# Performance work log

Measured on AMD Instinct MI355X. Metric: run time of the kernel, lower is better.

The kernel has to match this reference:

```python
import jax, jax.numpy as jnp
import numpy as np

EDGE_WIDTH = 64
NUM_HEADS = 8
DOT_DIM = EDGE_WIDTH // NUM_HEADS  # 8
B, N = 2, 384
LN_EPS = 1e-5


def setup_inputs() -> dict:
    key = jax.random.key(0)
    ks = jax.random.split(key, 8)
    e = jax.random.normal(ks[0], (B, N, N, EDGE_WIDTH), dtype=jnp.float32)
    mask = jnp.zeros((B, N, N, 1), dtype=jnp.float32)  # additive mask, broadcast over heads
    s = 1.0 / np.sqrt(EDGE_WIDTH)
    return {
        "e": e,
        "mask": mask,
        "ln_w": jnp.ones((EDGE_WIDTH,), jnp.float32),
        "ln_b": jnp.zeros((EDGE_WIDTH,), jnp.float32),
        "W_V": jax.random.normal(ks[1], (EDGE_WIDTH, 2 * EDGE_WIDTH), jnp.float32) * s,
        "b_V": jnp.zeros((2 * EDGE_WIDTH,), jnp.float32),
        "W_EG": jax.random.normal(ks[2], (EDGE_WIDTH, 4 * NUM_HEADS), jnp.float32) * s,
        "b_EG": jnp.zeros((4 * NUM_HEADS,), jnp.float32),
        "W_O": jax.random.normal(ks[3], (2 * EDGE_WIDTH, EDGE_WIDTH), jnp.float32) * (1.0 / np.sqrt(2 * EDGE_WIDTH)),
        "b_O": jnp.zeros((EDGE_WIDTH,), jnp.float32),
    }


def reference(e, mask, ln_w, ln_b, W_V, b_V, W_EG, b_EG, W_O, b_O):
    b, n = e.shape[0], e.shape[1]
    H, D = NUM_HEADS, DOT_DIM
    # LayerNorm over edge_width
    mu = jnp.mean(e, axis=-1, keepdims=True)
    var = jnp.mean(jnp.square(e - mu), axis=-1, keepdims=True)
    e_ln = (e - mu) * jax.lax.rsqrt(var + LN_EPS) * ln_w + ln_b

    V = e_ln @ W_V + b_V                        # [b,n,n,2*ew]
    V_in, V_out = jnp.split(V, 2, axis=-1)
    # view(..., dot_dim, num_heads): last dim splits with heads fastest
    V_in = V_in.reshape(b, n, n, D, H)
    V_out = V_out.reshape(b, n, n, D, H)

    EG = e_ln @ W_EG + b_EG                     # [b,n,n,4H]
    E_in, G_in, E_out, G_out = jnp.split(EG, 4, axis=-1)

    gates_in = jax.nn.sigmoid(G_in + mask)
    A_in = jax.nn.softmax(E_in + mask, axis=2) * gates_in      # [b,n,n,H]
    Va_in = jnp.einsum('bikh,bjkdh->bijdh', A_in, V_in)

    gates_out = jax.nn.sigmoid(G_out + mask)
    A_out = jax.nn.softmax(E_out + mask, axis=1) * gates_out   # [b,n,n,H]
    Va_out = jnp.einsum('bkih,bkjdh->bijdh', A_out, V_out)

    Va = jnp.concatenate([Va_in, Va_out], axis=-1).reshape(b, n, n, 2 * EDGE_WIDTH)
    return Va @ W_O + b_O
```

## Files before the change

### kernel.cpp

```cpp
#include <hip/hip_runtime.h>

#define N_ 384
#define LNEPS 1e-5f

typedef __attribute__((ext_vector_type(8))) short bf16x8;
typedef __attribute__((ext_vector_type(4))) float f32x4;

__device__ __forceinline__ float bf2f(unsigned int u) {
    union { unsigned int i; float f; } v; v.i = u << 16; return v.f;
}
__device__ __forceinline__ unsigned short f2bf(float f) {
    union { float f; unsigned int i; } v; v.f = f;
    return (unsigned short)((v.i + 0x7FFFu + ((v.i >> 16) & 1u)) >> 16);
}
__device__ __forceinline__ void gload16(const void* g, void* l) {
    __builtin_amdgcn_global_load_lds(
        (const __attribute__((address_space(1))) void*)g,
        (__attribute__((address_space(3))) void*)l, 16, 0, 0);
}

__global__ __launch_bounds__(256) void k0_prep(
    const float* __restrict__ W_V, const float* __restrict__ W_EG,
    unsigned short* __restrict__ Whi, unsigned short* __restrict__ Wlo)
{
    int x = blockIdx.x * 256 + threadIdx.x;
    if (x >= 10240) return;
    int col = x >> 6, k = x & 63;
    float wv = (col < 128) ? W_V[k * 128 + col] : W_EG[k * 32 + (col - 128)];
    unsigned short hi = f2bf(wv);
    Whi[x] = hi;
    Wlo[x] = f2bf(wv - bf2f(hi));
}

__global__ __launch_bounds__(256) void k1_ln_proj(
    const float* __restrict__ e, const float* __restrict__ mask,
    const float* __restrict__ ln_w, const float* __restrict__ ln_b,
    const unsigned short* __restrict__ Whi_g, const unsigned short* __restrict__ Wlo_g,
    const float* __restrict__ b_V, const float* __restrict__ b_EG,
    unsigned short* __restrict__ VtIn, unsigned short* __restrict__ VtOut,
    float* __restrict__ EGin, float* __restrict__ EGoutT)
{
    __shared__ __align__(16) char smem[25088];
    unsigned short* s_v = (unsigned short*)smem;
    float* s_eg = (float*)(smem + 16640);

    const int t = threadIdx.x;
    const int j0 = blockIdx.x * 4;
    const int i0 = blockIdx.y * 16;
    const int b  = blockIdx.z;

    const int l = t & 63, w = t >> 6;
    const int l15 = l & 15, lq = l >> 4;

    const int r = w * 16 + l15;
    const int r1f = i0 + (r >> 2), r2f = j0 + (r & 3);
    const float* erow = e + ((size_t)((b * N_ + r1f) * N_ + r2f)) * 64;
    float ev[16];
    {
        float4 e0 = *(const float4*)(erow + lq * 8);
        float4 e1 = *(const float4*)(erow + lq * 8 + 4);
        float4 e2 = *(const float4*)(erow + 32 + lq * 8);
        float4 e3 = *(const float4*)(erow + 32 + lq * 8 + 4);
        ev[0]=e0.x; ev[1]=e0.y; ev[2]=e0.z;  ev[3]=e0.w;
        ev[4]=e1.x; ev[5]=e1.y; ev[6]=e1.z;  ev[7]=e1.w;
        ev[8]=e2.x; ev[9]=e2.y; ev[10]=e2.z; ev[11]=e2.w;
        ev[12]=e3.x; ev[13]=e3.y; ev[14]=e3.z; ev[15]=e3.w;
    }
    float s = 0.f, sq = 0.f;
    #pragma unroll
    for (int j = 0; j < 16; ++j) { s += ev[j]; sq += ev[j] * ev[j]; }
    s  += __shfl_xor(s, 16);  s  += __shfl_xor(s, 32);
    sq += __shfl_xor(sq, 16); sq += __shfl_xor(sq, 32);
    const float mean = s * (1.f / 64.f);
    const float rstd = rsqrtf(sq * (1.f / 64.f) - mean * mean + LNEPS);

    bf16x8 ahi[2], alo[2];
    {
        float lnwv[16], lnbv[16];
        float4 w0 = *(const float4*)(ln_w + lq * 8);
        float4 w1 = *(const float4*)(ln_w + lq * 8 + 4);
        float4 w2 = *(const float4*)(ln_w + 32 + lq * 8);
        float4 w3 = *(const float4*)(ln_w + 32 + lq * 8 + 4);
        lnwv[0]=w0.x; lnwv[1]=w0.y; lnwv[2]=w0.z;  lnwv[3]=w0.w;
        lnwv[4]=w1.x; lnwv[5]=w1.y; lnwv[6]=w1.z;  lnwv[7]=w1.w;
        lnwv[8]=w2.x; lnwv[9]=w2.y; lnwv[10]=w2.z; lnwv[11]=w2.w;
        lnwv[12]=w3.x; lnwv[13]=w3.y; lnwv[14]=w3.z; lnwv[15]=w3.w;
        float4 b0 = *(const float4*)(ln_b + lq * 8);
        float4 b1 = *(const float4*)(ln_b + lq * 8 + 4);
        float4 b2 = *(const float4*)(ln_b + 32 + lq * 8);
        float4 b3 = *(const float4*)(ln_b + 32 + lq * 8 + 4);
        lnbv[0]=b0.x; lnbv[1]=b0.y; lnbv[2]=b0.z;  lnbv[3]=b0.w;
        lnbv[4]=b1.x; lnbv[5]=b1.y; lnbv[6]=b1.z;  lnbv[7]=b1.w;
        lnbv[8]=b2.x; lnbv[9]=b2.y; lnbv[10]=b2.z; lnbv[11]=b2.w;
        lnbv[12]=b3.x; lnbv[13]=b3.y; lnbv[14]=b3.z; lnbv[15]=b3.w;
        #pragma unroll
        for (int ks = 0; ks < 2; ++ks) {
            #pragma unroll
            for (int j = 0; j < 8; ++j) {
                float x = (ev[ks * 8 + j] - mean) * rstd * lnwv[ks * 8 + j] + lnbv[ks * 8 + j];
                unsigned short h = f2bf(x);
                unsigned short lo = f2bf(x - bf2f(h));
                ahi[ks][j] = (short)h;
                alo[ks][j] = (short)lo;
            }
        }
    }

    f32x4 acc[10];
    #pragma unroll
    for (int n = 0; n < 10; ++n) acc[n] = (f32x4){0.f, 0.f, 0.f, 0.f};

    #pragma unroll
    for (int n = 0; n < 10; ++n) {
        int brow = n * 16 + l15;
        const unsigned short* wh = Whi_g + brow * 64;
        bf16x8 bh0 = *(const bf16x8*)(wh + lq * 8);
        bf16x8 bh1 = *(const bf16x8*)(wh + 32 + lq * 8);
        acc[n] = __builtin_amdgcn_mfma_f32_16x16x32_bf16(ahi[0], bh0, acc[n], 0, 0, 0);
        acc[n] = __builtin_amdgcn_mfma_f32_16x16x32_bf16(ahi[1], bh1, acc[n], 0, 0, 0);
        acc[n] = __builtin_amdgcn_mfma_f32_16x16x32_bf16(alo[0], bh0, acc[n], 0, 0, 0);
        acc[n] = __builtin_amdgcn_mfma_f32_16x16x32_bf16(alo[1], bh1, acc[n], 0, 0, 0);
        if (n >= 8) {
            const unsigned short* wl = Wlo_g + brow * 64;
            bf16x8 bl0 = *(const bf16x8*)(wl + lq * 8);
            bf16x8 bl1 = *(const bf16x8*)(wl + 32 + lq * 8);
            acc[n] = __builtin_amdgcn_mfma_f32_16x16x32_bf16(ahi[0], bl0, acc[n], 0, 0, 0);
            acc[n] = __builtin_amdgcn_mfma_f32_16x16x32_bf16(ahi[1], bl1, acc[n], 0, 0, 0);
        }
    }

    #pragma unroll
    for (int n = 0; n < 8; ++n) {
        float bb = b_V[n * 16 + l15];
        #pragma unroll
        for (int q = 0; q < 4; ++q)
            s_v[(w * 16 + lq * 4 + q) * 130 + n * 16 + l15] = f2bf(acc[n][q] + bb);
    }
    #pragma unroll
    for (int n = 8; n < 10; ++n) {
        #pragma unroll
        for (int q = 0; q < 4; ++q)
            s_eg[(w * 16 + lq * 4 + q) * 33 + (n - 8) * 16 + l15] = acc[n][q];
    }
    __syncthreads();

    {
        const int rr = t & 63, g = t >> 6;
        const int r1 = i0 + (rr >> 2);
        const int r2 = j0 + (rr & 3);
        #pragma unroll
        for (int io = 0; io < 2; ++io) {
            #pragma unroll
            for (int hs = 0; hs < 2; ++hs) {
                const int h = g + hs * 4;
                uint4 u4;
                unsigned int wv[4];
                #pragma unroll
                for (int dp = 0; dp < 4; ++dp) {
                    int c0 = io * 64 + (2 * dp) * 8 + h;
                    int c1 = io * 64 + (2 * dp + 1) * 8 + h;
                    wv[dp] = (unsigned int)s_v[rr * 130 + c0]
                           | ((unsigned int)s_v[rr * 130 + c1] << 16);
                }
                u4.x = wv[0]; u4.y = wv[1]; u4.z = wv[2]; u4.w = wv[3];
                if (io == 0) {
                    *(uint4*)(VtIn + ((size_t)((b * 8 + h) * N_ + r2)) * 3072 + (size_t)r1 * 8) = u4;
                } else {
                    *(uint4*)(VtOut + ((size_t)((b * 8 + h) * N_ + r1)) * 3072 + (size_t)r2 * 8) = u4;
                }
            }
        }
    }
    {
        const int rr = t >> 2, cq = (t & 3) * 4;
        const int r1 = i0 + (rr >> 2);
        const int r2 = j0 + (rr & 3);
        const float maskv = mask[(size_t)(b * N_ + r1) * N_ + r2];
        float4 v0, v1;
        float tmp0[4], tmp1[4];
        #pragma unroll
        for (int u = 0; u < 4; ++u) {
            int c2 = cq + u;
            float x = s_eg[rr * 33 + c2] + b_EG[c2] + maskv;
            if (c2 >= 8) x = 1.f / (1.f + expf(-x));
            tmp0[u] = x;
            int c3 = 16 + cq + u;
            float y = s_eg[rr * 33 + c3] + b_EG[c3] + maskv;
            if ((cq + u) >= 8) y = 1.f / (1.f + expf(-y));
            tmp1[u] = y;
        }
        v0.x = tmp0[0]; v0.y = tmp0[1]; v0.z = tmp0[2]; v0.w = tmp0[3];
        v1.x = tmp1[0]; v1.y = tmp1[1]; v1.z = tmp1[2]; v1.w = tmp1[3];
        *(float4*)(EGin   + ((size_t)((b * N_ + r1) * N_ + r2)) * 16 + cq) = v0;
        *(float4*)(EGoutT + ((size_t)((b * N_ + r2) * N_ + r1)) * 16 + cq) = v1;
    }
}

__global__ __launch_bounds__(256) void k2m(
    const float* __restrict__ EGin, const float* __restrict__ EGoutT,
    unsigned short* __restrict__ A_in, unsigned short* __restrict__ A_outT)
{
    __shared__ float s[384 * 17];
    const int t = threadIdx.x;
    const int bid = blockIdx.x;
    const float* EG = (bid < 768) ? EGin : EGoutT;
    unsigned short* A = (bid < 768) ? A_in : A_outT;
    const int b2 = (bid < 768) ? bid : bid - 768;
    const int i = b2 % N_, b = b2 / N_;
    const float* base = EG + ((size_t)(b * N_ + i) * N_) * 16;
    for (int x = t; x < 6144; x += 256) {
        int k = x >> 4, c = x & 15;
        s[k * 17 + c] = base[x];
    }
    __syncthreads();
    const int h = t >> 5, l = t & 31;
    float ev[12];
    float mx = -1e30f;
    #pragma unroll
    for (int j = 0; j < 12; ++j) {
        ev[j] = s[(l + 32 * j) * 17 + h];
        mx = fmaxf(mx, ev[j]);
    }
    #pragma unroll
    for (int off = 16; off >= 1; off >>= 1) mx = fmaxf(mx, __shfl_xor(mx, off));
    float sum = 0.f;
    #pragma unroll
    for (int j = 0; j < 12; ++j) { ev[j] = expf(ev[j] - mx); sum += ev[j]; }
    #pragma unroll
    for (int off = 16; off >= 1; off >>= 1) sum += __shfl_xor(sum, off);
    const float inv = 1.f / sum;
    unsigned short* arow = A + ((size_t)((b * 8 + h) * N_ + i)) * N_;
    #pragma unroll
    for (int j = 0; j < 12; ++j) {
        int k = l + 32 * j;
        arow[k] = f2bf(ev[j] * inv * s[k * 17 + 8 + h]);
    }
}

__global__ __launch_bounds__(256) void k3_mfma(
    const unsigned short* __restrict__ Aall,
    const unsigned short* __restrict__ Vtall,
    unsigned short* __restrict__ C)
{
    __shared__ __align__(16) short sAB[17408];
    short* sA = sAB;
    unsigned short* sB = (unsigned short*)(sAB + 8192);

    const int t = threadIdx.x;
    const int n0 = blockIdx.x * 128;
    const int i0 = blockIdx.y * 128;
    const int z  = blockIdx.z;

    const unsigned short* Ap = Aall + (size_t)z * 147456;
    const unsigned short* Bp = Vtall + (size_t)z * 1179648;

    const int l = t & 63;
    const int w = t >> 6;
    const int wr = w >> 1, wc = w & 1;
    const int l15 = l & 15, lq = l >> 4;
    const int srow = l >> 3, schunk = (l & 7) ^ (l >> 3);

    f32x4 acc[4][4];
    #pragma unroll
    for (int mi = 0; mi < 4; ++mi)
        #pragma unroll
        for (int ni = 0; ni < 4; ++ni) acc[mi][ni] = (f32x4){0.f, 0.f, 0.f, 0.f};

    #pragma unroll 1
    for (int kt = 0; kt < 6; ++kt) {
        const int k0 = kt * 64;
        #pragma unroll
        for (int i = 0; i < 4; ++i) {
            int rbase = w * 32 + i * 8;
            gload16(Ap + (size_t)(i0 + rbase + srow) * 384 + k0 + schunk * 8,
                    (char*)sA + rbase * 128);
        }
        #pragma unroll
        for (int rep = 0; rep < 4; ++rep) {
            int flat = rep * 256 + t;
            int kk = flat >> 4;
            int o  = flat & 15;
            uint4 v = *(const uint4*)(Bp + (size_t)(k0 + kk) * 3072 + n0 + o * 8);
            int cc = ((kk >> 3) ^ o) & 7;
            int base = (o * 8) * 72 + cc * 8 + (kk & 7);
            sB[base]       = (unsigned short)(v.x);
            sB[base + 72]  = (unsigned short)(v.x >> 16);
            sB[base + 144] = (unsigned short)(v.y);
            sB[base + 216] = (unsigned short)(v.y >> 16);
            sB[base + 288] = (unsigned short)(v.z);
            sB[base + 360] = (unsigned short)(v.z >> 16);
            sB[base + 432] = (unsigned short)(v.w);
            sB[base + 504] = (unsigned short)(v.w >> 16);
        }
        __syncthreads();

        bf16x8 av[4][2], bv[4][2];
        #pragma unroll
        for (int mi = 0; mi < 4; ++mi) {
            int row = wr * 64 + mi * 16 + l15;
            #pragma unroll
            for (int ks = 0; ks < 2; ++ks) {
                int kc = ks * 4 + lq;
                av[mi][ks] = *(const bf16x8*)((const char*)sA + row * 128 + ((kc ^ (row & 7)) << 4));
            }
        }
        #pragma unroll
        for (int ni = 0; ni < 4; ++ni) {
            int jd = wc * 64 + ni * 16 + l15;
            #pragma unroll
            for (int ks = 0; ks < 2; ++ks) {
                int c = ks * 4 + lq;
                int cc = (c ^ ((jd >> 3) & 7)) & 7;
                bv[ni][ks] = *(const bf16x8*)((const char*)sB + (jd * 72 + cc * 8) * 2);
            }
        }
        #pragma unroll
        for (int mi = 0; mi < 4; ++mi)
            #pragma unroll
            for (int ni = 0; ni < 4; ++ni) {
                acc[mi][ni] = __builtin_amdgcn_mfma_f32_16x16x32_bf16(av[mi][0], bv[ni][0], acc[mi][ni], 0, 0, 0);
                acc[mi][ni] = __builtin_amdgcn_mfma_f32_16x16x32_bf16(av[mi][1], bv[ni][1], acc[mi][ni], 0, 0, 0);
            }
        __syncthreads();
    }

    unsigned short* Cp = C + (size_t)z * 1179648;
    #pragma unroll
    for (int mi = 0; mi < 4; ++mi) {
        #pragma unroll
        for (int qq = 0; qq < 4; ++qq) {
            int row = i0 + wr * 64 + mi * 16 + lq * 4 + qq;
            unsigned short* crow = Cp + (size_t)row * 3072 + n0 + wc * 64 + l15;
            #pragma unroll
            for (int ni = 0; ni < 4; ++ni) crow[ni * 16] = f2bf(acc[mi][ni][qq]);
        }
    }
}

__global__ __launch_bounds__(256) void k4_proj(
    const unsigned short* __restrict__ C, const float* __restrict__ W_O,
    const float* __restrict__ b_O, float* __restrict__ out)
{
    __shared__ float s_w[8192];
    __shared__ unsigned short s_c[20480];
    const int t = threadIdx.x;
    const int jt = blockIdx.x;
    const int i  = blockIdx.y;
    const int b  = blockIdx.z;

    for (int x = t; x < 8192; x += 256) s_w[x] = W_O[x];
    {
        unsigned int* s_c32 = (unsigned int*)s_c;
        #pragma unroll
        for (int rep = 0; rep < 8; ++rep) {
            int flat = rep * 256 + t;
            int p = flat >> 7, jj = flat & 127;
            int plane = b * 8 + (p & 7) + (p >> 3) * 16;
            uint4 v = *(const uint4*)(C + (size_t)plane * 1179648 + (size_t)i * 3072 + jt * 1024 + jj * 8);
            int base = p * 640 + jj * 5;
            s_c32[base] = v.x; s_c32[base + 1] = v.y; s_c32[base + 2] = v.z; s_c32[base + 3] = v.w;
        }
    }
    __syncthreads();

    const int jg = t & 63, cg = t >> 6;
    const int chb = cg * 16;
    float acc0[16], acc1[16];
    #pragma unroll
    for (int u = 0; u < 16; ++u) { float bb = b_O[chb + u]; acc0[u] = bb; acc1[u] = bb; }

    #pragma unroll 4
    for (int c = 0; c < 128; ++c) {
        const int p = c & 15, d = c >> 4;
        const int sbase = p * 1280 + (jg * 2) * 10 + d;
        float v0 = bf2f((unsigned int)s_c[sbase]);
        float v1 = bf2f((unsigned int)s_c[sbase + 10]);
        const float* wrp = s_w + c * 64 + chb;
        #pragma unroll
        for (int u4 = 0; u4 < 4; ++u4) {
            float4 wv = *(const float4*)(wrp + u4 * 4);
            acc0[u4*4+0] += v0 * wv.x; acc0[u4*4+1] += v0 * wv.y;
            acc0[u4*4+2] += v0 * wv.z; acc0[u4*4+3] += v0 * wv.w;
            acc1[u4*4+0] += v1 * wv.x; acc1[u4*4+1] += v1 * wv.y;
            acc1[u4*4+2] += v1 * wv.z; acc1[u4*4+3] += v1 * wv.w;
        }
    }
    float* o0 = out + ((size_t)(b * N_ + i) * N_ + jt * 128 + jg * 2) * 64 + chb;
    #pragma unroll
    for (int u4 = 0; u4 < 4; ++u4) {
        float4 a; a.x = acc0[u4*4]; a.y = acc0[u4*4+1]; a.z = acc0[u4*4+2]; a.w = acc0[u4*4+3];
        *(float4*)(o0 + u4 * 4) = a;
        float4 c4; c4.x = acc1[u4*4]; c4.y = acc1[u4*4+1]; c4.z = acc1[u4*4+2]; c4.w = acc1[u4*4+3];
        *(float4*)(o0 + 64 + u4 * 4) = c4;
    }
}

extern "C" void kernel_launch(void* const* d_in, const int* in_sizes, int n_in,
                              void* d_out, int out_size, void* d_ws, size_t ws_size,
                              hipStream_t stream)
{
    const float* e    = (const float*)d_in[0];
    const float* mask = (const float*)d_in[1];
    const float* ln_w = (const float*)d_in[2];
    const float* ln_b = (const float*)d_in[3];
    const float* W_V  = (const float*)d_in[4];
    const float* b_V  = (const float*)d_in[5];
    const float* W_EG = (const float*)d_in[6];
    const float* b_EG = (const float*)d_in[7];
    const float* W_O  = (const float*)d_in[8];
    const float* b_O  = (const float*)d_in[9];
    float* out = (float*)d_out;

    char* ws = (char*)d_ws;
    unsigned short* VtIn   = (unsigned short*)(ws);
    unsigned short* VtOut  = (unsigned short*)(ws + 37748736);
    unsigned short* A_in   = (unsigned short*)(ws + 75497472);
    unsigned short* A_outT = (unsigned short*)(ws + 80216064);
    float* EGin   = (float*)(ws + 84934656);
    float* EGoutT = (float*)(ws + 103809024);
    unsigned short* Cws    = (unsigned short*)(ws + 84934656);
    unsigned short* Whi = A_in;
    unsigned short* Wlo = A_in + 10240;

    hipLaunchKernelGGL(k0_prep, dim3(40), dim3(256), 0, stream, W_V, W_EG, Whi, Wlo);
    hipLaunchKernelGGL(k1_ln_proj, dim3(96, 24, 2), dim3(256), 0, stream,
                       e, mask, ln_w, ln_b, Whi, Wlo, b_V, b_EG, VtIn, VtOut, EGin, EGoutT);
    hipLaunchKernelGGL(k2m, dim3(1536), dim3(256), 0, stream,
                       EGin, EGoutT, A_in, A_outT);
    hipLaunchKernelGGL(k3_mfma, dim3(24, 3, 32), dim3(256), 0, stream,
                       A_in, VtIn, Cws);
    hipLaunchKernelGGL(k4_proj, dim3(3, 384, 2), dim3(256), 0, stream,
                       Cws, W_O, b_O, out);
}
```

Before: 240.5 us.

## Use bf16 MFMA with hi/lo split for output projection and swizzle k3 grid

The final W_O projection kernel moves from scalar fp32 FMAs over LDS-staged weights to bf16 MFMA. W_O is pre-split into hi/lo bf16 halves in the prep kernel to keep accuracy close to fp32, and the weight fragments are read straight from global memory. The C tile is transposed into LDS so it can feed the MFMA A operand. Separately, the batched MFMA kernel now uses a 1D grid with an XCD-style swizzle to group blocks that share data, which adds index arithmetic and changes block ordering.

```diff
diff --git a/kernel.cpp b/kernel.cpp
--- a/kernel.cpp
+++ b/kernel.cpp
@@ -21,15 +21,25 @@
 
 __global__ __launch_bounds__(256) void k0_prep(
     const float* __restrict__ W_V, const float* __restrict__ W_EG,
-    unsigned short* __restrict__ Whi, unsigned short* __restrict__ Wlo)
+    const float* __restrict__ W_O,
+    unsigned short* __restrict__ Whi, unsigned short* __restrict__ Wlo,
+    unsigned short* __restrict__ WoHi, unsigned short* __restrict__ WoLo)
 {
     int x = blockIdx.x * 256 + threadIdx.x;
-    if (x >= 10240) return;
-    int col = x >> 6, k = x & 63;
-    float wv = (col < 128) ? W_V[k * 128 + col] : W_EG[k * 32 + (col - 128)];
-    unsigned short hi = f2bf(wv);
-    Whi[x] = hi;
-    Wlo[x] = f2bf(wv - bf2f(hi));
+    if (x < 10240) {
+        int col = x >> 6, k = x & 63;
+        float wv = (col < 128) ? W_V[k * 128 + col] : W_EG[k * 32 + (col - 128)];
+        unsigned short hi = f2bf(wv);
+        Whi[x] = hi;
+        Wlo[x] = f2bf(wv - bf2f(hi));
+    } else if (x < 18432) {
+        int y = x - 10240;
+        int cout = y >> 7, c = y & 127;
+        float wv = W_O[c * 64 + cout];
+        unsigned short hi = f2bf(wv);
+        WoHi[y] = hi;
+        WoLo[y] = f2bf(wv - bf2f(hi));
+    }
 }
 
 __global__ __launch_bounds__(256) void k1_ln_proj(
@@ -247,9 +257,12 @@
     unsigned short* sB = (unsigned short*)(sAB + 8192);
 
     const int t = threadIdx.x;
-    const int n0 = blockIdx.x * 128;
-    const int i0 = blockIdx.y * 128;
-    const int z  = blockIdx.z;
+    const int flat = blockIdx.x;
+    const int swz = (flat & 7) * 288 + (flat >> 3);
+    const int z  = swz / 72;
+    const int rem = swz % 72;
+    const int i0 = (rem / 24) * 128;
+    const int n0 = (rem % 24) * 128;
 
     const unsigned short* Ap = Aall + (size_t)z * 147456;
     const unsigned short* Bp = Vtall + (size_t)z * 1179648;
@@ -277,9 +290,9 @@
         }
         #pragma unroll
         for (int rep = 0; rep < 4; ++rep) {
-            int flat = rep * 256 + t;
-            int kk = flat >> 4;
-            int o  = flat & 15;
+            int flat2 = rep * 256 + t;
+            int kk = flat2 >> 4;
+            int o  = flat2 & 15;
             uint4 v = *(const uint4*)(Bp + (size_t)(k0 + kk) * 3072 + n0 + o * 8);
             int cc = ((kk >> 3) ^ o) & 7;
             int base = (o * 8) * 72 + cc * 8 + (kk & 7);
@@ -338,60 +351,72 @@
 }
 
 __global__ __launch_bounds__(256) void k4_proj(
-    const unsigned short* __restrict__ C, const float* __restrict__ W_O,
+    const unsigned short* __restrict__ C,
+    const unsigned short* __restrict__ WoHi, const unsigned short* __restrict__ WoLo,
     const float* __restrict__ b_O, float* __restrict__ out)
 {
-    __shared__ float s_w[8192];
-    __shared__ unsigned short s_c[20480];
+    __shared__ __align__(16) unsigned short s_ct[128 * 136];
     const int t = threadIdx.x;
     const int jt = blockIdx.x;
     const int i  = blockIdx.y;
     const int b  = blockIdx.z;
 
-    for (int x = t; x < 8192; x += 256) s_w[x] = W_O[x];
-    {
-        unsigned int* s_c32 = (unsigned int*)s_c;
-        #pragma unroll
-        for (int rep = 0; rep < 8; ++rep) {
-            int flat = rep * 256 + t;
-            int p = flat >> 7, jj = flat & 127;
-            int plane = b * 8 + (p & 7) + (p >> 3) * 16;
-            uint4 v = *(const uint4*)(C + (size_t)plane * 1179648 + (size_t)i * 3072 + jt * 1024 + jj * 8);
-            int base = p * 640 + jj * 5;
-            s_c32[base] = v.x; s_c32[base + 1] = v.y; s_c32[base + 2] = v.z; s_c32[base + 3] = v.w;
-        }
+    #pragma unroll
+    for (int rep = 0; rep < 8; ++rep) {
+        int flat = rep * 256 + t;
+        int p = flat >> 7, jj = flat & 127;
+        int plane = b * 8 + (p & 7) + (p >> 3) * 16;
+        uint4 v = *(const uint4*)(C + (size_t)plane * 1179648 + (size_t)i * 3072 + jt * 1024 + jj * 8);
+        unsigned short* dst = s_ct + jj * 136 + p;
+        dst[0]   = (unsigned short)(v.x);
+        dst[16]  = (unsigned short)(v.x >> 16);
+        dst[32]  = (unsigned short)(v.y);
+        dst[48]  = (unsigned short)(v.y >> 16);
+        dst[64]  = (unsigned short)(v.z);
+        dst[80]  = (unsigned short)(v.z >> 16);
+        dst[96]  = (unsigned short)(v.w);
+        dst[112] = (unsigned short)(v.w >> 16);
     }
     __syncthreads();
 
-    const int jg = t & 63, cg = t >> 6;
-    const int chb = cg * 16;
-    float acc0[16], acc1[16];
-    #pragma unroll
-    for (int u = 0; u < 16; ++u) { float bb = b_O[chb + u]; acc0[u] = bb; acc1[u] = bb; }
-
-    #pragma unroll 4
-    for (int c = 0; c < 128; ++c) {
-        const int p = c & 15, d = c >> 4;
-        const int sbase = p * 1280 + (jg * 2) * 10 + d;
-        float v0 = bf2f((unsigned int)s_c[sbase]);
-        float v1 = bf2f((unsigned int)s_c[sbase + 10]);
-        const float* wrp = s_w + c * 64 + chb;
-        #pragma unroll
-        for (int u4 = 0; u4 < 4; ++u4) {
-            float4 wv = *(const float4*)(wrp + u4 * 4);
-            acc0[u4*4+0] += v0 * wv.x; acc0[u4*4+1] += v0 * wv.y;
-            acc0[u4*4+2] += v0 * wv.z; acc0[u4*4+3] += v0 * wv.w;
-            acc1[u4*4+0] += v1 * wv.x; acc1[u4*4+1] += v1 * wv.y;
-            acc1[u4*4+2] += v1 * wv.z; acc1[u4*4+3] += v1 * wv.w;
-        }
-    }
-    float* o0 = out + ((size_t)(b * N_ + i) * N_ + jt * 128 + jg * 2) * 64 + chb;
-    #pragma unroll
-    for (int u4 = 0; u4 < 4; ++u4) {
-        float4 a; a.x = acc0[u4*4]; a.y = acc0[u4*4+1]; a.z = acc0[u4*4+2]; a.w = acc0[u4*4+3];
-        *(float4*)(o0 + u4 * 4) = a;
-        float4 c4; c4.x = acc1[u4*4]; c4.y = acc1[u4*4+1]; c4.z = acc1[u4*4+2]; c4.w = acc1[u4*4+3];
-        *(float4*)(o0 + 64 + u4 * 4) = c4;
+    const int l = t & 63, w = t >> 6;
+    const int l15 = l & 15, lq = l >> 4;
+
+    f32x4 acc[2][4];
+    #pragma unroll
+    for (int m = 0; m < 2; ++m)
+        #pragma unroll
+        for (int nt = 0; nt < 4; ++nt) {
+            float bb = b_O[nt * 16 + l15];
+            acc[m][nt] = (f32x4){bb, bb, bb, bb};
+        }
+
+    #pragma unroll
+    for (int ks = 0; ks < 4; ++ks) {
+        bf16x8 av0 = *(const bf16x8*)(s_ct + (w * 32 + l15) * 136 + ks * 32 + lq * 8);
+        bf16x8 av1 = *(const bf16x8*)(s_ct + (w * 32 + 16 + l15) * 136 + ks * 32 + lq * 8);
+        #pragma unroll
+        for (int nt = 0; nt < 4; ++nt) {
+            bf16x8 bh = *(const bf16x8*)(WoHi + (nt * 16 + l15) * 128 + ks * 32 + lq * 8);
+            bf16x8 bl = *(const bf16x8*)(WoLo + (nt * 16 + l15) * 128 + ks * 32 + lq * 8);
+            acc[0][nt] = __builtin_amdgcn_mfma_f32_16x16x32_bf16(av0, bh, acc[0][nt], 0, 0, 0);
+            acc[0][nt] = __builtin_amdgcn_mfma_f32_16x16x32_bf16(av0, bl, acc[0][nt], 0, 0, 0);
+            acc[1][nt] = __builtin_amdgcn_mfma_f32_16x16x32_bf16(av1, bh, acc[1][nt], 0, 0, 0);
+            acc[1][nt] = __builtin_amdgcn_mfma_f32_16x16x32_bf16(av1, bl, acc[1][nt], 0, 0, 0);
+        }
+    }
+
+    #pragma unroll
+    for (int m = 0; m < 2; ++m) {
+        #pragma unroll
+        for (int q = 0; q < 4; ++q) {
+            int j = w * 32 + m * 16 + lq * 4 + q;
+            float* orow = out + ((size_t)(b * N_ + i) * N_ + jt * 128 + j) * 64 + l15;
+            orow[0]  = acc[m][0][q];
+            orow[16] = acc[m][1][q];
+            orow[32] = acc[m][2][q];
+            orow[48] = acc[m][3][q];
+        }
     }
 }
 
@@ -421,14 +446,17 @@
     unsigned short* Cws    = (unsigned short*)(ws + 84934656);
     unsigned short* Whi = A_in;
     unsigned short* Wlo = A_in + 10240;
-
-    hipLaunchKernelGGL(k0_prep, dim3(40), dim3(256), 0, stream, W_V, W_EG, Whi, Wlo);
+    unsigned short* WoHi = (unsigned short*)(ws + 160432128);
+    unsigned short* WoLo = (unsigned short*)(ws + 160448512);
+
+    hipLaunchKernelGGL(k0_prep, dim3(72), dim3(256), 0, stream,
+                       W_V, W_EG, W_O, Whi, Wlo, WoHi, WoLo);
     hipLaunchKernelGGL(k1_ln_proj, dim3(96, 24, 2), dim3(256), 0, stream,
                        e, mask, ln_w, ln_b, Whi, Wlo, b_V, b_EG, VtIn, VtOut, EGin, EGoutT);
     hipLaunchKernelGGL(k2m, dim3(1536), dim3(256), 0, stream,
                        EGin, EGoutT, A_in, A_outT);
-    hipLaunchKernelGGL(k3_mfma, dim3(24, 3, 32), dim3(256), 0, stream,
+    hipLaunchKernelGGL(k3_mfma, dim3(2304), dim3(256), 0, stream,
                        A_in, VtIn, Cws);
     hipLaunchKernelGGL(k4_proj, dim3(3, 384, 2), dim3(256), 0, stream,
-                       Cws, W_O, b_O, out);
-}
+                       Cws, WoHi, WoLo, b_O, out);
+}
```

After: 215.3 us. -10.5%, faster.
